# Performance work log

Hardware: AMD Instinct MI355X
Metric: run time of the kernel (lower is better)

## Reference

```python
import jax, jax.numpy as jnp
import numpy as np

WS = 7        # kernel_size
DIL = 1       # dilation
HEADS = 8


def _reflect(idx, L):
    # stnls-style reflect bounds (no edge duplication): -1 -> 1, L -> L-2
    period = 2 * (L - 1)
    m = jnp.mod(idx, period)
    return jnp.where(m > L - 1, period - m, m)


def setup_inputs() -> dict:
    key = jax.random.key(0)
    k1, k2, k3 = jax.random.split(key, 3)
    T, H, W, C = 8, 64, 64, 256
    x = jax.random.normal(k1, (T, H, W, C), jnp.float32)
    # flows: (1, T, 2*wt, 2, H, W) with wt=1; channel 0 = di (rows), 1 = dj (cols)
    flows = jax.random.normal(k2, (1, T, 2, 2, H, W), jnp.float32) * 2.0
    W_qk = jax.random.normal(k3, (2 * C, C), jnp.float32) * 0.02
    return {"x": x, "flows": flows, "W_qk": W_qk}


def _slot(q, k, tp, fli, flj):
    # q,k: (HD,T,H,W,hd); tp: (T,) frame index per query frame; fli,flj: (T,H,W) flow
    HD, T, H, W, hd = q.shape
    di = jnp.round(fli).astype(jnp.int32)   # itype='int': integer flow offsets
    dj = jnp.round(flj).astype(jnp.int32)
    ci = jnp.arange(H, dtype=jnp.int32)[None, :, None] + di   # (T,H,W) window centers
    cj = jnp.arange(W, dtype=jnp.int32)[None, None, :] + dj
    kg = k[:, tp]                                             # (HD,T,H,W,hd) keys of searched frame
    off = DIL * (jnp.arange(WS, dtype=jnp.int32) - WS // 2)
    t_idx = jnp.arange(T)[:, None, None, None]
    ii = jnp.arange(H, dtype=jnp.int32)[None, :, None]
    jj = jnp.arange(W, dtype=jnp.int32)[None, None, :, None]
    dt = (tp - jnp.arange(T)).astype(jnp.int32)               # (T,)
    scores, offs = [], []
    for a in range(WS):  # structural loop over window rows to bound intermediates
        li = _reflect(ci + off[a], H)                                    # (T,H,W)
        lj = _reflect(cj[..., None] + off[None, None, None, :], W)       # (T,H,W,WS)
        kn = kg[:, t_idx, li[..., None], lj, :]                          # (HD,T,H,W,WS,hd)
        scores.append(jnp.einsum('dthwf,dthwbf->dthwb', q, kn))         # (HD,T,H,W,WS)
        o = jnp.stack([
            jnp.broadcast_to(dt[:, None, None, None], (T, H, W, WS)),
            jnp.broadcast_to((li - ii[:, :, :]) [..., None], (T, H, W, WS)),
            lj - jj], axis=-1)                                           # (T,H,W,WS,3)
        offs.append(o)
    s = jnp.stack(scores, axis=4).reshape(HD, T, H, W, WS * WS)
    o = jnp.stack(offs, axis=3).reshape(T, H, W, WS * WS, 3)
    return s, o


def reference(x, flows, W_qk):
    T, H, W, C = x.shape
    hd = C // HEADS
    scale = hd ** (-0.5)
    qk = (x @ W_qk.T).reshape(T, H, W, 2, HEADS, hd)
    q = jnp.transpose(qk[:, :, :, 0], (3, 0, 1, 2, 4))  # (HD,T,H,W,hd)
    k = jnp.transpose(qk[:, :, :, 1], (3, 0, 1, 2, 4))
    t = jnp.arange(T)
    tp1 = jnp.where(t + 1 < T, t + 1, t - 2)   # forward frame, window shifted at boundary
    tp2 = jnp.where(t - 1 >= 0, t - 1, t + 2)  # backward frame
    z = jnp.zeros((T, H, W), x.dtype)
    s0, o0 = _slot(q, k, t, z, z)
    s1, o1 = _slot(q, k, tp1, flows[0, :, 0, 0], flows[0, :, 0, 1])
    s2, o2 = _slot(q, k, tp2, flows[0, :, 1, 0], flows[0, :, 1, 1])
    attn = scale * jnp.concatenate([s0, s1, s2], axis=-1)[None]   # (1,HD,T,H,W,K)
    fk = jnp.concatenate([o0, o1, o2], axis=3)                    # (T,H,W,K,3)
    flows_k = jnp.broadcast_to(fk[None, None], (1, HEADS) + fk.shape)
    return attn, flows_k
```

## Files before the change

### kernel.cpp

```cpp
#include <hip/hip_runtime.h>
#include <hip/hip_bf16.h>

#define TT_    8
#define HEADS_ 8
#define NB_    147
#define NPIX   32768
#define NTASK  (NPIX*NB_)
#define ROWS_  (NPIX + 512)

typedef _Float16 half8 __attribute__((ext_vector_type(8)));
typedef _Float16 h2    __attribute__((ext_vector_type(2)));
typedef float    f32x4 __attribute__((ext_vector_type(4)));

__device__ __forceinline__ int reflect64(int v) {
  int m = v % 126;
  m += (m >> 31) & 126;
  return (m > 63) ? (126 - m) : m;
}

__device__ __forceinline__ float dot2f(h2 a, h2 b, float c) {
#if __has_builtin(__builtin_amdgcn_fdot2)
  return __builtin_amdgcn_fdot2(a, b, c, false);
#else
  return c + (float)a[0]*(float)b[0] + (float)a[1]*(float)b[1];
#endif
}

__global__ __launch_bounds__(256) void prepack(
    const float* __restrict__ x, const float* __restrict__ wqk,
    _Float16* __restrict__ outp) {
  int o  = (int)blockIdx.x * 256 + (int)threadIdx.x;
  int r  = o & 15, quad = (o >> 4) & 3, ks = (o >> 6) & 7, mt = o >> 9;
  int row = mt * 16 + r;
  const float* src = (row < NPIX) ? (x + (size_t)row * 256)
                                  : (wqk + (size_t)(row - NPIX) * 256);
  int col = (ks * 4 + quad) * 8;
  float4 a = *(const float4*)(src + col);
  float4 b = *(const float4*)(src + col + 4);
  half8 h;
  h[0]=(_Float16)a.x; h[1]=(_Float16)a.y; h[2]=(_Float16)a.z; h[3]=(_Float16)a.w;
  h[4]=(_Float16)b.x; h[5]=(_Float16)b.y; h[6]=(_Float16)b.z; h[7]=(_Float16)b.w;
  ((half8*)outp)[o] = h;
}

__global__ __launch_bounds__(256) void qk_gemm(
    const _Float16* __restrict__ Ap,
    _Float16* __restrict__ qws, _Float16* __restrict__ kws) {
  const half8* A8 = (const half8*)Ap;
  const half8* B8 = (const half8*)(Ap + (size_t)NPIX * 256);
  int bid  = (int)blockIdx.x;
  int mblk = bid >> 3, nblk = bid & 7;
  int lane = (int)threadIdx.x & 63, wv = (int)threadIdx.x >> 6;
  int wm = mblk * 64 + (wv >> 1) * 32;
  int wn = nblk * 64 + (wv & 1) * 32;
  int r = lane & 15, quad = lane >> 4;

  half8 af[2][8], bf[2][8];
#pragma unroll
  for (int im = 0; im < 2; im++) {
    int mt = (wm >> 4) + im;
#pragma unroll
    for (int ks = 0; ks < 8; ks++)
      af[im][ks] = A8[((mt * 8 + ks) * 4 + quad) * 16 + r];
  }
#pragma unroll
  for (int in = 0; in < 2; in++) {
    int nt = (wn >> 4) + in;
#pragma unroll
    for (int ks = 0; ks < 8; ks++)
      bf[in][ks] = B8[((nt * 8 + ks) * 4 + quad) * 16 + r];
  }

  f32x4 acc[2][2] = {};
#pragma unroll
  for (int ks = 0; ks < 8; ks++)
#pragma unroll
    for (int im = 0; im < 2; im++)
#pragma unroll
      for (int in = 0; in < 2; in++)
        acc[im][in] = __builtin_amdgcn_mfma_f32_16x16x32_f16(
            af[im][ks], bf[in][ks], acc[im][in], 0, 0, 0);

  _Float16* dst = (wn < 256) ? qws : kws;
  int nsub = (wn < 256) ? 0 : 256;
#pragma unroll
  for (int im = 0; im < 2; im++)
#pragma unroll
    for (int in = 0; in < 2; in++) {
      int n = wn + in * 16 + r - nsub;
#pragma unroll
      for (int reg = 0; reg < 4; reg++) {
        int m = wm + im * 16 + quad * 4 + reg;
        dst[(size_t)m * 256 + n] = (_Float16)acc[im][in][reg];
      }
    }
}

__global__ __launch_bounds__(256) void attn_kernel(
    const float* __restrict__ flows,
    const _Float16* __restrict__ qws, const _Float16* __restrict__ kws,
    float* __restrict__ out) {
  __shared__ int      s_info[256];
  __shared__ __attribute__((aligned(16))) _Float16 s_q[3 * 4 * 8 * 8];
  __shared__ __attribute__((aligned(16))) float    s_attn[8 * 260];
  __shared__ __attribute__((aligned(16))) float    s_flow[768];

  int nbq = (int)gridDim.x >> 3;
  int blk = ((int)blockIdx.x & 7) * nbq + ((int)blockIdx.x >> 3);
  int tx  = (int)threadIdx.x;
  int btid0 = blk * 256;
  int p0 = (int)((unsigned)btid0 / 147u);

  {
    int tid = btid0 + tx;
    unsigned p = (unsigned)tid / 147u;
    int nb = tid - (int)(p * 147u);
    int t = (int)(p >> 12), hw = (int)(p & 4095u);
    int h = hw >> 6, w = hw & 63;
    int slot = nb / 49;
    int rr = nb - slot * 49;
    int a = rr / 7, b = rr - a * 7;
    int tp = t, di = 0, dj = 0;
    if (slot > 0) {
      int si = slot - 1;
      di = (int)rintf(flows[(size_t)((t * 2 + si) * 2 + 0) * 4096 + hw]);
      dj = (int)rintf(flows[(size_t)((t * 2 + si) * 2 + 1) * 4096 + hw]);
      tp = (slot == 1) ? ((t + 1 < TT_) ? t + 1 : t - 2)
                       : ((t - 1 >= 0)  ? t - 1 : t + 2);
    }
    int li = reflect64(h + di + a - 3);
    int lj = reflect64(w + dj + b - 3);
    int kidx = (tp << 12) + (li << 6) + lj;
    int pixloc = (int)p - p0;
    s_info[tx] = kidx | (pixloc << 20);
    s_flow[tx * 3 + 0] = (float)(tp - t);
    s_flow[tx * 3 + 1] = (float)(li - h);
    s_flow[tx * 3 + 2] = (float)(lj - w);
  }
  if (tx < 96) {
    int pix = tx >> 5, s = tx & 31;
    int p = p0 + pix; if (p > NPIX - 1) p = NPIX - 1;
    half8 v = *(const half8*)(qws + (size_t)p * 256 + s * 8);
    ((half8*)s_q)[(pix * 4 + (s & 3)) * 8 + (s >> 2)] = v;
  }
  __syncthreads();

  int lane = tx & 63, wv = tx >> 6;
  int j = lane & 7, g = lane >> 3;
  const float scale = 0.17677669529663687f;
#pragma unroll
  for (int it = 0; it < 8; it++) {
    int tb = wv * 64 + it * 8 + g;
    int info = s_info[tb];
    int kidx = info & 0xFFFFF;
    int pixloc = info >> 20;
    const _Float16* kv = kws + (size_t)kidx * 256 + j * 32;
    float s = 0.f;
#pragma unroll
    for (int c = 0; c < 4; c++) {
      half8 k8 = *(const half8*)(kv + c * 8);
      half8 q8 = ((const half8*)s_q)[(pixloc * 4 + c) * 8 + j];
#pragma unroll
      for (int u = 0; u < 8; u += 2) {
        h2 ka = { k8[u], k8[u + 1] };
        h2 qa = { q8[u], q8[u + 1] };
        s = dot2f(ka, qa, s);
      }
    }
    s_attn[j * 260 + tb] = s * scale;
  }
  __syncthreads();

  const float4* sa4 = (const float4*)s_attn;
#pragma unroll
  for (int o = 0; o < 2; o++) {
    int gg = tx + o * 256;
    int hh = gg >> 6, idx = gg & 63;
    ((float4*)(out + (size_t)hh * NTASK + btid0))[idx] = sa4[hh * 65 + idx];
  }
  float* fo = out + (size_t)HEADS_ * NTASK;
  const float4* sf4 = (const float4*)s_flow;
#pragma unroll
  for (int o = 0; o < 6; o++) {
    int gg = tx + o * 256;
    int hh = gg / 192, idx = gg - hh * 192;
    ((float4*)(fo + (size_t)hh * NTASK * 3 + (size_t)btid0 * 3))[idx] = sf4[idx];
  }
}

extern "C" void kernel_launch(void* const* d_in, const int* in_sizes, int n_in,
                              void* d_out, int out_size, void* d_ws, size_t ws_size,
                              hipStream_t stream) {
  const float* x     = (const float*)d_in[0];
  const float* flows = (const float*)d_in[1];
  const float* wqk   = (const float*)d_in[2];
  float* out = (float*)d_out;

  _Float16* qws = (_Float16*)d_ws;
  _Float16* kws = qws + (size_t)NPIX * 256;
  _Float16* Ap  = kws + (size_t)NPIX * 256;

  prepack<<<dim3(ROWS_ * 32 / 256), dim3(256), 0, stream>>>(x, wqk, Ap);
  qk_gemm<<<dim3(4096), dim3(256), 0, stream>>>(Ap, qws, kws);
  attn_kernel<<<dim3(NTASK / 256), dim3(256), 0, stream>>>(flows, qws, kws, out);
}
```

Baseline: 769.2 us.

## Coalesce key loads across lanes with DPP head reduction and nontemporal stores

Each group of 8 lanes now reads one contiguous 256-element key row, lane j taking chunk j of each 64-element block, so the group's loads are coalesced instead of each lane reading its own 32-element head slice. The partial dot products are then combined across groups of 4 lanes with DPP xor shuffles, and one lane per quad writes the head score. The Q shared-memory layout is changed to match. Output stores are made nontemporal to keep the large write-only output from polluting the cache. This adds shuffle instructions and some divergent stores.

```diff
diff --git a/kernel.cpp b/kernel.cpp
--- a/kernel.cpp
+++ b/kernel.cpp
@@ -24,6 +24,15 @@
 #else
   return c + (float)a[0]*(float)b[0] + (float)a[1]*(float)b[1];
 #endif
+}
+
+__device__ __forceinline__ float dpp_xor1(float x) {
+  int r = __builtin_amdgcn_mov_dpp(__builtin_bit_cast(int, x), 0xB1, 0xF, 0xF, true);
+  return __builtin_bit_cast(float, r);
+}
+__device__ __forceinline__ float dpp_xor2(float x) {
+  int r = __builtin_amdgcn_mov_dpp(__builtin_bit_cast(int, x), 0x4E, 0xF, 0xF, true);
+  return __builtin_bit_cast(float, r);
 }
 
 __global__ __launch_bounds__(256) void prepack(
@@ -101,7 +110,7 @@
     const _Float16* __restrict__ qws, const _Float16* __restrict__ kws,
     float* __restrict__ out) {
   __shared__ int      s_info[256];
-  __shared__ __attribute__((aligned(16))) _Float16 s_q[3 * 4 * 8 * 8];
+  __shared__ __attribute__((aligned(16))) _Float16 s_q[3 * 32 * 8];
   __shared__ __attribute__((aligned(16))) float    s_attn[8 * 260];
   __shared__ __attribute__((aligned(16))) float    s_flow[768];
 
@@ -141,7 +150,7 @@
     int pix = tx >> 5, s = tx & 31;
     int p = p0 + pix; if (p > NPIX - 1) p = NPIX - 1;
     half8 v = *(const half8*)(qws + (size_t)p * 256 + s * 8);
-    ((half8*)s_q)[(pix * 4 + (s & 3)) * 8 + (s >> 2)] = v;
+    ((half8*)s_q)[pix * 32 + s] = v;
   }
   __syncthreads();
 
@@ -154,37 +163,49 @@
     int info = s_info[tb];
     int kidx = info & 0xFFFFF;
     int pixloc = info >> 20;
-    const _Float16* kv = kws + (size_t)kidx * 256 + j * 32;
-    float s = 0.f;
+    const half8* kp = (const half8*)(kws + ((size_t)kidx << 8)) + j;
+    const half8* qp = ((const half8*)s_q) + pixloc * 32 + j;
+    float acc[4];
 #pragma unroll
     for (int c = 0; c < 4; c++) {
-      half8 k8 = *(const half8*)(kv + c * 8);
-      half8 q8 = ((const half8*)s_q)[(pixloc * 4 + c) * 8 + j];
+      half8 k8 = kp[c * 8];
+      half8 q8 = qp[c * 8];
+      float s = 0.f;
 #pragma unroll
       for (int u = 0; u < 8; u += 2) {
         h2 ka = { k8[u], k8[u + 1] };
         h2 qa = { q8[u], q8[u + 1] };
         s = dot2f(ka, qa, s);
       }
-    }
-    s_attn[j * 260 + tb] = s * scale;
+      acc[c] = s;
+    }
+#pragma unroll
+    for (int c = 0; c < 4; c++) {
+      float t = acc[c];
+      t += dpp_xor1(t);
+      t += dpp_xor2(t);
+      if ((lane & 3) == 0)
+        s_attn[(2 * c + ((lane >> 2) & 1)) * 260 + tb] = t * scale;
+    }
   }
   __syncthreads();
 
-  const float4* sa4 = (const float4*)s_attn;
+  const f32x4* sa4 = (const f32x4*)s_attn;
 #pragma unroll
   for (int o = 0; o < 2; o++) {
     int gg = tx + o * 256;
     int hh = gg >> 6, idx = gg & 63;
-    ((float4*)(out + (size_t)hh * NTASK + btid0))[idx] = sa4[hh * 65 + idx];
+    f32x4 v = sa4[hh * 65 + idx];
+    __builtin_nontemporal_store(v, (f32x4*)(out + (size_t)hh * NTASK + btid0) + idx);
   }
   float* fo = out + (size_t)HEADS_ * NTASK;
-  const float4* sf4 = (const float4*)s_flow;
+  const f32x4* sf4 = (const f32x4*)s_flow;
 #pragma unroll
   for (int o = 0; o < 6; o++) {
     int gg = tx + o * 256;
     int hh = gg / 192, idx = gg - hh * 192;
-    ((float4*)(fo + (size_t)hh * NTASK * 3 + (size_t)btid0 * 3))[idx] = sf4[idx];
+    f32x4 v = sf4[idx];
+    __builtin_nontemporal_store(v, (f32x4*)(fo + (size_t)hh * NTASK * 3 + (size_t)btid0 * 3) + idx);
   }
 }
 
```

New measurement: 680.5 us. 1.13x faster.
